# Optimization experiments

Measured on AMD Instinct MI355X. Metric: run time of the kernel, lower is better.

Reference implementation:

```python
import jax, jax.numpy as jnp
import numpy as np

ALPHA = 0.1
NUM_CLASSES = 1000
B, D = 16384, 2048


def setup_inputs() -> dict:
    key = jax.random.key(0)
    k1, k2 = jax.random.split(key)
    x = jax.random.normal(k1, (B, D), dtype=jnp.float32)
    y = jax.random.randint(k2, (B,), 0, NUM_CLASSES)
    return {"x": x, "y": y}


def reference(x, y):
    # Per-class mean/std via a single segment reduction (equivalent to the
    # original masked loop over classes; torch .std(0) is unbiased, ddof=1).
    cnt = jax.ops.segment_sum(jnp.ones((x.shape[0],), x.dtype), y, num_segments=NUM_CLASSES)  # [C]
    s = jax.ops.segment_sum(x, y, num_segments=NUM_CLASSES)        # [C, D]
    sq = jax.ops.segment_sum(x * x, y, num_segments=NUM_CLASSES)   # [C, D]
    cnt_ = cnt[:, None]
    mean = s / cnt_
    var = (sq - cnt_ * mean * mean) / (cnt_ - 1.0)  # unbiased variance
    std = jnp.sqrt(jnp.maximum(var, 0.0))
    nk, pk = jax.random.split(jax.random.key(42))
    # torch.normal(mean, std).detach()
    class_noise = jax.lax.stop_gradient(mean + std * jax.random.normal(nk, mean.shape, x.dtype))
    index = jax.random.permutation(pk, x.shape[0])
    newY = y[index]
    out = (1.0 - ALPHA) * x + ALPHA * class_noise[newY]
    return out, newY
```

## Files before the change

kernel.cpp:

```cpp
#include <hip/hip_runtime.h>
#include <cstdint>
#include <cstddef>

#define B_ROWS 16384
#define D_COLS 2048
#define NCLS   1000
#define NBUCK  1024

typedef float f4v __attribute__((ext_vector_type(4)));

__device__ __forceinline__ void nt_store_f4(float4* p, float4 v) {
    __builtin_nontemporal_store(*reinterpret_cast<f4v*>(&v),
                                reinterpret_cast<f4v*>(p));
}

__host__ __device__ __forceinline__ uint32_t rotl32(uint32_t v, int r) {
    return (v << r) | (v >> (32 - r));
}

__host__ __device__ inline void tf2x32(uint32_t k0, uint32_t k1,
                                       uint32_t x0, uint32_t x1,
                                       uint32_t& o0, uint32_t& o1) {
    uint32_t ks0 = k0, ks1 = k1, ks2 = k0 ^ k1 ^ 0x1BD11BDAu;
    x0 += ks0; x1 += ks1;
    x0 += x1; x1 = rotl32(x1, 13); x1 ^= x0;
    x0 += x1; x1 = rotl32(x1, 15); x1 ^= x0;
    x0 += x1; x1 = rotl32(x1, 26); x1 ^= x0;
    x0 += x1; x1 = rotl32(x1, 6);  x1 ^= x0;
    x0 += ks1; x1 += ks2 + 1u;
    x0 += x1; x1 = rotl32(x1, 17); x1 ^= x0;
    x0 += x1; x1 = rotl32(x1, 29); x1 ^= x0;
    x0 += x1; x1 = rotl32(x1, 16); x1 ^= x0;
    x0 += x1; x1 = rotl32(x1, 24); x1 ^= x0;
    x0 += ks2; x1 += ks0 + 2u;
    x0 += x1; x1 = rotl32(x1, 13); x1 ^= x0;
    x0 += x1; x1 = rotl32(x1, 15); x1 ^= x0;
    x0 += x1; x1 = rotl32(x1, 26); x1 ^= x0;
    x0 += x1; x1 = rotl32(x1, 6);  x1 ^= x0;
    x0 += ks0; x1 += ks1 + 3u;
    x0 += x1; x1 = rotl32(x1, 17); x1 ^= x0;
    x0 += x1; x1 = rotl32(x1, 29); x1 ^= x0;
    x0 += x1; x1 = rotl32(x1, 16); x1 ^= x0;
    x0 += x1; x1 = rotl32(x1, 24); x1 ^= x0;
    x0 += ks1; x1 += ks2 + 4u;
    x0 += x1; x1 = rotl32(x1, 13); x1 ^= x0;
    x0 += x1; x1 = rotl32(x1, 15); x1 ^= x0;
    x0 += x1; x1 = rotl32(x1, 26); x1 ^= x0;
    x0 += x1; x1 = rotl32(x1, 6);  x1 ^= x0;
    x0 += ks2; x1 += ks0 + 5u;
    o0 = x0; o1 = x1;
}

__device__ __forceinline__ float erfinv_f(float x) {
    float w = -log1pf(-x * x);
    float p;
    if (w < 5.0f) {
        w -= 2.5f;
        p = 2.81022636e-08f;
        p = fmaf(p, w, 3.43273939e-07f);
        p = fmaf(p, w, -3.5233877e-06f);
        p = fmaf(p, w, -4.39150654e-06f);
        p = fmaf(p, w, 0.00021858087f);
        p = fmaf(p, w, -0.00125372503f);
        p = fmaf(p, w, -0.00417768164f);
        p = fmaf(p, w, 0.246640727f);
        p = fmaf(p, w, 1.50140941f);
    } else {
        w = sqrtf(w) - 3.0f;
        p = -0.000200214257f;
        p = fmaf(p, w, 0.000100950558f);
        p = fmaf(p, w, 0.00134934322f);
        p = fmaf(p, w, -0.00367342844f);
        p = fmaf(p, w, 0.00573950773f);
        p = fmaf(p, w, -0.0076224613f);
        p = fmaf(p, w, 0.00943887047f);
        p = fmaf(p, w, 1.00167406f);
        p = fmaf(p, w, 2.83297682f);
    }
    return p * x;
}


__global__ void k_bits_hist(const int* __restrict__ y, int* __restrict__ cnt,
                            uint32_t* __restrict__ kAbits, uint32_t* __restrict__ kBbits,
                            int* __restrict__ bhA, int* __restrict__ bhB,
                            uint32_t s1_0, uint32_t s1_1,
                            uint32_t s2_0, uint32_t s2_1) {
    int i = blockIdx.x * 256 + threadIdx.x;
    atomicAdd(&cnt[y[i]], 1);
    uint32_t a, b;
    tf2x32(s1_0, s1_1, 0u, (uint32_t)i, a, b);
    uint32_t bitsA = a ^ b;
    kAbits[i] = bitsA;
    atomicAdd(&bhA[bitsA >> 22], 1);
    tf2x32(s2_0, s2_1, 0u, (uint32_t)i, a, b);
    uint32_t bitsB = a ^ b;
    kBbits[i] = bitsB;
    atomicAdd(&bhB[bitsB >> 22], 1);
}

__global__ void k_prefix3(const int* __restrict__ cnt, int* __restrict__ rowstart,
                          const int* __restrict__ bhA, int* __restrict__ bsA,
                          const int* __restrict__ bhB, int* __restrict__ bsB) {
    __shared__ int sm[1024];
    int t = threadIdx.x;
    const int* src; int* dst; int n;
    if (blockIdx.x == 0)      { src = cnt; dst = rowstart; n = NCLS; }
    else if (blockIdx.x == 1) { src = bhA; dst = bsA;      n = NBUCK; }
    else                      { src = bhB; dst = bsB;      n = NBUCK; }
    int v = (t < n) ? src[t] : 0;
    sm[t] = v;
    for (int off = 1; off < 1024; off <<= 1) {
        __syncthreads();
        int u = (t >= off) ? sm[t - off] : 0;
        __syncthreads();
        sm[t] += u;
    }
    if (t < n) dst[t] = sm[t] - v;
}

__global__ void k_scatter_all(const int* __restrict__ y,
                              const uint32_t* __restrict__ kAbits,
                              const uint32_t* __restrict__ kBbits,
                              const int* __restrict__ rowstart, int* __restrict__ rowpos,
                              int* __restrict__ rowlist,
                              const int* __restrict__ bsA, int* __restrict__ bposA,
                              int* __restrict__ memA,
                              const int* __restrict__ bsB, int* __restrict__ bposB,
                              int* __restrict__ memB) {
    int i = blockIdx.x * 256 + threadIdx.x;
    int c = y[i];
    int p = atomicAdd(&rowpos[c], 1);
    rowlist[rowstart[c] + p] = i;
    uint32_t bA = kAbits[i] >> 22;
    p = atomicAdd(&bposA[bA], 1);
    memA[bsA[bA] + p] = i;
    uint32_t bB = kBbits[i] >> 22;
    p = atomicAdd(&bposB[bB], 1);
    memB[bsB[bB] + p] = i;
}

__global__ void __launch_bounds__(256) k_mid(
        const float* __restrict__ x, const int* __restrict__ rowlist,
        const int* __restrict__ rowstart, const int* __restrict__ cnt,
        float* __restrict__ noise, uint32_t nk0, uint32_t nk1,
        const uint32_t* __restrict__ kAbits, const uint32_t* __restrict__ kBbits,
        const int* __restrict__ bsA, const int* __restrict__ bhA,
        const int* __restrict__ memA,
        const int* __restrict__ bsB, const int* __restrict__ bhB,
        const int* __restrict__ memB,
        int* __restrict__ x1, int* __restrict__ rank2) {
    int bid = blockIdx.x, t = threadIdx.x;
    if (bid >= 64) {
        int cb = bid - 64;
        int c = cb >> 1, h = cb & 1;
        int start = rowstart[c], n = cnt[c];
        const float4* xb = (const float4*)x + (size_t)h * 256 + t;
        float sx=0,sy=0,sz=0,sw=0, qx=0,qy=0,qz=0,qw=0;
        int r = 0;
        for (; r + 2 <= n; r += 2) {
            int row0 = rowlist[start + r];
            int row1 = rowlist[start + r + 1];
            float4 a = xb[(size_t)row0 * 512];
            float4 b = xb[(size_t)row1 * 512];
            sx += a.x; sy += a.y; sz += a.z; sw += a.w;
            qx = fmaf(a.x, a.x, qx); qy = fmaf(a.y, a.y, qy);
            qz = fmaf(a.z, a.z, qz); qw = fmaf(a.w, a.w, qw);
            sx += b.x; sy += b.y; sz += b.z; sw += b.w;
            qx = fmaf(b.x, b.x, qx); qy = fmaf(b.y, b.y, qy);
            qz = fmaf(b.z, b.z, qz); qw = fmaf(b.w, b.w, qw);
        }
        if (r < n) {
            int row = rowlist[start + r];
            float4 a = xb[(size_t)row * 512];
            sx += a.x; sy += a.y; sz += a.z; sw += a.w;
            qx = fmaf(a.x, a.x, qx); qy = fmaf(a.y, a.y, qy);
            qz = fmaf(a.z, a.z, qz); qw = fmaf(a.w, a.w, qw);
        }
        float sarr[4] = {sx, sy, sz, sw};
        float qarr[4] = {qx, qy, qz, qw};
        float oarr[4];
        float cf = (float)n;
        uint32_t nbase = (uint32_t)(c * 2048 + h * 1024 + t * 4);
        #pragma unroll
        for (int j = 0; j < 4; ++j) {
            uint32_t b1, b2;
            tf2x32(nk0, nk1, 0u, nbase + (uint32_t)j, b1, b2);
            uint32_t bits = b1 ^ b2;
            float f = __uint_as_float((bits >> 9) | 0x3f800000u) - 1.0f;
            const float LO = -0.99999994f;
            float u = fmaxf(LO, fmaf(f, 2.0f, LO));
            float nrm = 1.41421356f * erfinv_f(u);
            float m = sarr[j] / cf;
            float var = (qarr[j] - cf * m * m) / (cf - 1.0f);
            float sd = sqrtf(fmaxf(var, 0.0f));
            oarr[j] = fmaf(sd, nrm, m);
        }
        int o = c * 512 + h * 256 + t;
        ((float4*)noise)[o] = make_float4(oarr[0], oarr[1], oarr[2], oarr[3]);
    } else {
        int i = bid * 256 + t;
        uint32_t a = kAbits[i];
        {
            uint32_t b = a >> 22;
            int st = bsA[b], n = bhA[b];
            int ca = 0;
            for (int k = 0; k < n; k++) {
                int m = memA[st + k];
                uint32_t mb = kAbits[m];
                ca += (mb < a) || (mb == a && m < i);
            }
            x1[st + ca] = i;
        }
        uint32_t c = kBbits[i];
        {
            uint32_t b = c >> 22;
            int st = bsB[b], n = bhB[b];
            int cb = 0;
            for (int k = 0; k < n; k++) {
                int m = memB[st + k];
                uint32_t mb = kBbits[m];
                cb += (mb < c) || (mb == c && m < i);
            }
            rank2[i] = st + cb;
        }
    }
}

__global__ void k_scatter2(const int* __restrict__ y, const int* __restrict__ x1,
                           const int* __restrict__ rank2, int* __restrict__ newY,
                           float* __restrict__ outTail) {
    int i = blockIdx.x * 256 + threadIdx.x;
    int v = y[x1[i]];
    int j = rank2[i];
    newY[j] = v;
    outTail[j] = (float)v;
}

__global__ void __launch_bounds__(256) k_final(
        const float* __restrict__ x, const float* __restrict__ noise,
        const int* __restrict__ newY, float* __restrict__ out) {
    int b = blockIdx.x, t = threadIdx.x;
    int ny = newY[b];
    const float4* xr = (const float4*)x + (size_t)b * (D_COLS / 4);
    const float4* nr = (const float4*)noise + (size_t)ny * (D_COLS / 4);
    float4* orow = (float4*)out + (size_t)b * (D_COLS / 4);
    float4 xa = xr[t], na = nr[t];
    float4 o;
    o.x = fmaf(0.1f, na.x, 0.9f * xa.x);
    o.y = fmaf(0.1f, na.y, 0.9f * xa.y);
    o.z = fmaf(0.1f, na.z, 0.9f * xa.z);
    o.w = fmaf(0.1f, na.w, 0.9f * xa.w);
    nt_store_f4(&orow[t], o);
    xa = xr[t + 256]; na = nr[t + 256];
    o.x = fmaf(0.1f, na.x, 0.9f * xa.x);
    o.y = fmaf(0.1f, na.y, 0.9f * xa.y);
    o.z = fmaf(0.1f, na.z, 0.9f * xa.z);
    o.w = fmaf(0.1f, na.w, 0.9f * xa.w);
    nt_store_f4(&orow[t + 256], o);
}

extern "C" void kernel_launch(void* const* d_in, const int* in_sizes, int n_in,
                              void* d_out, int out_size, void* d_ws, size_t ws_size,
                              hipStream_t stream) {
    const float* x = (const float*)d_in[0];
    const int* y = (const int*)d_in[1];
    float* out = (float*)d_out;
    float* outTail = out + (size_t)B_ROWS * D_COLS;

    char* ws = (char*)d_ws;
    float* noise = (float*)(ws + 16384000);
    int* ints = (int*)(ws + 24576000);
    int* cnt      = ints;
    int* rowpos   = ints + 1000;
    int* bhA      = ints + 2000;
    int* bposA    = ints + 3024;
    int* bhB      = ints + 4048;
    int* bposB    = ints + 5072;
    int* rowstart = ints + 6096;
    int* bsA      = ints + 7096;
    int* bsB      = ints + 8120;
    int* rowlist  = ints + 9144;
    int* memA     = ints + 25528;
    int* memB     = ints + 41912;
    int* x1       = ints + 58296;
    int* rank2    = ints + 74680;
    int* newY     = ints + 91064;
    uint32_t* kAbits = (uint32_t*)(ints + 107448);
    uint32_t* kBbits = (uint32_t*)(ints + 123832);

    hipMemsetAsync(cnt, 0, 6096 * sizeof(int), stream);

    uint32_t nk0, nk1, pk0, pk1, pn0, pn1, s1_0, s1_1, s2_0, s2_1;
    tf2x32(0u, 42u, 0u, 0u, nk0, nk1);
    tf2x32(0u, 42u, 0u, 1u, pk0, pk1);
    tf2x32(pk0, pk1, 0u, 0u, pn0, pn1);
    tf2x32(pk0, pk1, 0u, 1u, s1_0, s1_1);
    tf2x32(pn0, pn1, 0u, 1u, s2_0, s2_1);

    k_bits_hist<<<64, 256, 0, stream>>>(y, cnt, kAbits, kBbits, bhA, bhB,
                                        s1_0, s1_1, s2_0, s2_1);
    k_prefix3<<<3, 1024, 0, stream>>>(cnt, rowstart, bhA, bsA, bhB, bsB);
    k_scatter_all<<<64, 256, 0, stream>>>(y, kAbits, kBbits, rowstart, rowpos,
                                          rowlist, bsA, bposA, memA,
                                          bsB, bposB, memB);
    k_mid<<<2 * NCLS + 64, 256, 0, stream>>>(x, rowlist, rowstart, cnt,
                                             noise, nk0, nk1,
                                             kAbits, kBbits,
                                             bsA, bhA, memA,
                                             bsB, bhB, memB, x1, rank2);
    k_scatter2<<<64, 256, 0, stream>>>(y, x1, rank2, newY, outTail);
    k_final<<<16384, 256, 0, stream>>>(x, noise, newY, out);
}
```

Baseline: 299.5 us.

## Fuse front-end histogram/prefix/scatter via grid barrier and merge scatter2 into final

Merges the histogram, prefix-scan and scatter kernels into one 64-block kernel that uses a software grid barrier built on agent-scope atomics. The prefix scan now runs with 256 threads handling four elements each. The newY scatter kernel is folded into the final blend kernel, which writes each output row directly at its permuted destination. This removes three kernel launches and one intermediate buffer, but relies on all 64 blocks being co-resident for the spin barrier to avoid deadlock.

```diff
diff --git a/kernel.cpp b/kernel.cpp
--- a/kernel.cpp
+++ b/kernel.cpp
@@ -12,6 +12,26 @@
 __device__ __forceinline__ void nt_store_f4(float4* p, float4 v) {
     __builtin_nontemporal_store(*reinterpret_cast<f4v*>(&v),
                                 reinterpret_cast<f4v*>(p));
+}
+
+__device__ __forceinline__ void gbar(int* slot, int nblk) {
+    __syncthreads();
+    if (threadIdx.x == 0) {
+        __threadfence();
+        int v = __hip_atomic_fetch_add(&slot[0], 1, __ATOMIC_ACQ_REL,
+                                       __HIP_MEMORY_SCOPE_AGENT);
+        if (v == nblk - 1) {
+            __hip_atomic_store(&slot[1], 1, __ATOMIC_RELEASE,
+                               __HIP_MEMORY_SCOPE_AGENT);
+        } else {
+            while (__hip_atomic_load(&slot[1], __ATOMIC_ACQUIRE,
+                                     __HIP_MEMORY_SCOPE_AGENT) == 0) {
+                __builtin_amdgcn_s_sleep(1);
+            }
+        }
+        __threadfence();
+    }
+    __syncthreads();
 }
 
 __host__ __device__ __forceinline__ uint32_t rotl32(uint32_t v, int r) {
@@ -81,13 +101,21 @@
 }
 
 
-__global__ void k_bits_hist(const int* __restrict__ y, int* __restrict__ cnt,
-                            uint32_t* __restrict__ kAbits, uint32_t* __restrict__ kBbits,
-                            int* __restrict__ bhA, int* __restrict__ bhB,
-                            uint32_t s1_0, uint32_t s1_1,
-                            uint32_t s2_0, uint32_t s2_1) {
-    int i = blockIdx.x * 256 + threadIdx.x;
-    atomicAdd(&cnt[y[i]], 1);
+__global__ void __launch_bounds__(256) k_front(
+        const int* __restrict__ y, int* __restrict__ cnt,
+        uint32_t* __restrict__ kAbits, uint32_t* __restrict__ kBbits,
+        int* __restrict__ bhA, int* __restrict__ bhB,
+        int* __restrict__ rowstart, int* __restrict__ rowpos,
+        int* __restrict__ rowlist,
+        int* __restrict__ bsA, int* __restrict__ bposA, int* __restrict__ memA,
+        int* __restrict__ bsB, int* __restrict__ bposB, int* __restrict__ memB,
+        int* __restrict__ bar,
+        uint32_t s1_0, uint32_t s1_1, uint32_t s2_0, uint32_t s2_1) {
+    int t = threadIdx.x, bid = blockIdx.x;
+    int i = bid * 256 + t;
+
+    int yi = y[i];
+    atomicAdd(&cnt[yi], 1);
     uint32_t a, b;
     tf2x32(s1_0, s1_1, 0u, (uint32_t)i, a, b);
     uint32_t bitsA = a ^ b;
@@ -97,45 +125,44 @@
     uint32_t bitsB = a ^ b;
     kBbits[i] = bitsB;
     atomicAdd(&bhB[bitsB >> 22], 1);
-}
-
-__global__ void k_prefix3(const int* __restrict__ cnt, int* __restrict__ rowstart,
-                          const int* __restrict__ bhA, int* __restrict__ bsA,
-                          const int* __restrict__ bhB, int* __restrict__ bsB) {
-    __shared__ int sm[1024];
-    int t = threadIdx.x;
-    const int* src; int* dst; int n;
-    if (blockIdx.x == 0)      { src = cnt; dst = rowstart; n = NCLS; }
-    else if (blockIdx.x == 1) { src = bhA; dst = bsA;      n = NBUCK; }
-    else                      { src = bhB; dst = bsB;      n = NBUCK; }
-    int v = (t < n) ? src[t] : 0;
-    sm[t] = v;
-    for (int off = 1; off < 1024; off <<= 1) {
+
+    gbar(bar + 0, 64);
+
+    if (bid < 3) {
+        const int* src; int* dst; int n;
+        if (bid == 0)      { src = cnt; dst = rowstart; n = NCLS; }
+        else if (bid == 1) { src = bhA; dst = bsA;      n = NBUCK; }
+        else               { src = bhB; dst = bsB;      n = NBUCK; }
+        __shared__ int sm[256];
+        int base = t * 4;
+        int v0 = (base + 0 < n) ? src[base + 0] : 0;
+        int v1 = (base + 1 < n) ? src[base + 1] : 0;
+        int v2 = (base + 2 < n) ? src[base + 2] : 0;
+        int v3 = (base + 3 < n) ? src[base + 3] : 0;
+        int s01 = v0 + v1, s012 = s01 + v2, sall = s012 + v3;
+        sm[t] = sall;
+        for (int off = 1; off < 256; off <<= 1) {
+            __syncthreads();
+            int u = (t >= off) ? sm[t - off] : 0;
+            __syncthreads();
+            sm[t] += u;
+        }
         __syncthreads();
-        int u = (t >= off) ? sm[t - off] : 0;
-        __syncthreads();
-        sm[t] += u;
+        int excl = sm[t] - sall;
+        if (base + 0 < n) dst[base + 0] = excl;
+        if (base + 1 < n) dst[base + 1] = excl + v0;
+        if (base + 2 < n) dst[base + 2] = excl + s01;
+        if (base + 3 < n) dst[base + 3] = excl + s012;
     }
-    if (t < n) dst[t] = sm[t] - v;
-}
-
-__global__ void k_scatter_all(const int* __restrict__ y,
-                              const uint32_t* __restrict__ kAbits,
-                              const uint32_t* __restrict__ kBbits,
-                              const int* __restrict__ rowstart, int* __restrict__ rowpos,
-                              int* __restrict__ rowlist,
-                              const int* __restrict__ bsA, int* __restrict__ bposA,
-                              int* __restrict__ memA,
-                              const int* __restrict__ bsB, int* __restrict__ bposB,
-                              int* __restrict__ memB) {
-    int i = blockIdx.x * 256 + threadIdx.x;
-    int c = y[i];
-    int p = atomicAdd(&rowpos[c], 1);
-    rowlist[rowstart[c] + p] = i;
-    uint32_t bA = kAbits[i] >> 22;
+
+    gbar(bar + 2, 64);
+
+    int p = atomicAdd(&rowpos[yi], 1);
+    rowlist[rowstart[yi] + p] = i;
+    uint32_t bA = bitsA >> 22;
     p = atomicAdd(&bposA[bA], 1);
     memA[bsA[bA] + p] = i;
-    uint32_t bB = kBbits[i] >> 22;
+    uint32_t bB = bitsB >> 22;
     p = atomicAdd(&bposB[bB], 1);
     memB[bsB[bB] + p] = i;
 }
@@ -227,24 +254,18 @@
     }
 }
 
-__global__ void k_scatter2(const int* __restrict__ y, const int* __restrict__ x1,
-                           const int* __restrict__ rank2, int* __restrict__ newY,
-                           float* __restrict__ outTail) {
-    int i = blockIdx.x * 256 + threadIdx.x;
+__global__ void __launch_bounds__(256) k_final2(
+        const float* __restrict__ x, const float* __restrict__ noise,
+        const int* __restrict__ y, const int* __restrict__ x1,
+        const int* __restrict__ rank2,
+        float* __restrict__ out, float* __restrict__ outTail) {
+    int i = blockIdx.x, t = threadIdx.x;
+    int j = rank2[i];
     int v = y[x1[i]];
-    int j = rank2[i];
-    newY[j] = v;
-    outTail[j] = (float)v;
-}
-
-__global__ void __launch_bounds__(256) k_final(
-        const float* __restrict__ x, const float* __restrict__ noise,
-        const int* __restrict__ newY, float* __restrict__ out) {
-    int b = blockIdx.x, t = threadIdx.x;
-    int ny = newY[b];
-    const float4* xr = (const float4*)x + (size_t)b * (D_COLS / 4);
-    const float4* nr = (const float4*)noise + (size_t)ny * (D_COLS / 4);
-    float4* orow = (float4*)out + (size_t)b * (D_COLS / 4);
+    if (t == 0) outTail[j] = (float)v;
+    const float4* xr = (const float4*)x + (size_t)j * (D_COLS / 4);
+    const float4* nr = (const float4*)noise + (size_t)v * (D_COLS / 4);
+    float4* orow = (float4*)out + (size_t)j * (D_COLS / 4);
     float4 xa = xr[t], na = nr[t];
     float4 o;
     o.x = fmaf(0.1f, na.x, 0.9f * xa.x);
@@ -271,25 +292,25 @@
     char* ws = (char*)d_ws;
     float* noise = (float*)(ws + 16384000);
     int* ints = (int*)(ws + 24576000);
-    int* cnt      = ints;
-    int* rowpos   = ints + 1000;
-    int* bhA      = ints + 2000;
-    int* bposA    = ints + 3024;
-    int* bhB      = ints + 4048;
-    int* bposB    = ints + 5072;
-    int* rowstart = ints + 6096;
-    int* bsA      = ints + 7096;
-    int* bsB      = ints + 8120;
-    int* rowlist  = ints + 9144;
-    int* memA     = ints + 25528;
-    int* memB     = ints + 41912;
-    int* x1       = ints + 58296;
-    int* rank2    = ints + 74680;
-    int* newY     = ints + 91064;
-    uint32_t* kAbits = (uint32_t*)(ints + 107448);
-    uint32_t* kBbits = (uint32_t*)(ints + 123832);
-
-    hipMemsetAsync(cnt, 0, 6096 * sizeof(int), stream);
+    int* bar      = ints;
+    int* cnt      = ints + 8;
+    int* rowpos   = ints + 1008;
+    int* bhA      = ints + 2008;
+    int* bposA    = ints + 3032;
+    int* bhB      = ints + 4056;
+    int* bposB    = ints + 5080;
+    int* rowstart = ints + 6104;
+    int* bsA      = ints + 7104;
+    int* bsB      = ints + 8128;
+    int* rowlist  = ints + 9152;
+    int* memA     = ints + 25536;
+    int* memB     = ints + 41920;
+    int* x1       = ints + 58304;
+    int* rank2    = ints + 74688;
+    uint32_t* kAbits = (uint32_t*)(ints + 91072);
+    uint32_t* kBbits = (uint32_t*)(ints + 107456);
+
+    hipMemsetAsync(ints, 0, 6104 * sizeof(int), stream);
 
     uint32_t nk0, nk1, pk0, pk1, pn0, pn1, s1_0, s1_1, s2_0, s2_1;
     tf2x32(0u, 42u, 0u, 0u, nk0, nk1);
@@ -298,17 +319,14 @@
     tf2x32(pk0, pk1, 0u, 1u, s1_0, s1_1);
     tf2x32(pn0, pn1, 0u, 1u, s2_0, s2_1);
 
-    k_bits_hist<<<64, 256, 0, stream>>>(y, cnt, kAbits, kBbits, bhA, bhB,
-                                        s1_0, s1_1, s2_0, s2_1);
-    k_prefix3<<<3, 1024, 0, stream>>>(cnt, rowstart, bhA, bsA, bhB, bsB);
-    k_scatter_all<<<64, 256, 0, stream>>>(y, kAbits, kBbits, rowstart, rowpos,
-                                          rowlist, bsA, bposA, memA,
-                                          bsB, bposB, memB);
+    k_front<<<64, 256, 0, stream>>>(y, cnt, kAbits, kBbits, bhA, bhB,
+                                    rowstart, rowpos, rowlist,
+                                    bsA, bposA, memA, bsB, bposB, memB,
+                                    bar, s1_0, s1_1, s2_0, s2_1);
     k_mid<<<2 * NCLS + 64, 256, 0, stream>>>(x, rowlist, rowstart, cnt,
                                              noise, nk0, nk1,
                                              kAbits, kBbits,
                                              bsA, bhA, memA,
                                              bsB, bhB, memB, x1, rank2);
-    k_scatter2<<<64, 256, 0, stream>>>(y, x1, rank2, newY, outTail);
-    k_final<<<16384, 256, 0, stream>>>(x, noise, newY, out);
-}
+    k_final2<<<16384, 256, 0, stream>>>(x, noise, y, x1, rank2, out, outTail);
+}
```

Result: no change. 305.2 us (+1.9%).
